# Performance work log

Measured on AMD Instinct MI355X. Metric: run time of the kernel, lower is better.

## Reference

```python
import jax, jax.numpy as jnp
import numpy as np

B, C, H, W = 8, 96, 96, 96
K = 3          # attn_kernels == kernels
HK = 3         # hidden_kernels
NORM_SCALE = 1.0
EPS = 1e-5


def conv2d_same(x, w):
    # x: [B,Cin,H,W], w: [Cout,Cin,k,k], same padding (k odd)
    k = w.shape[-1]
    p = k // 2
    return jax.lax.conv_general_dilated(
        x, w, window_strides=(1, 1), padding=((p, p), (p, p)),
        dimension_numbers=("NCHW", "OIHW", "NCHW"))


def batchnorm_train(x):
    # torch BatchNorm2d (affine=False), training-mode: biased var over (B,H,W)
    mu = jnp.mean(x, axis=(0, 2, 3), keepdims=True)
    var = jnp.var(x, axis=(0, 2, 3), keepdims=True)
    return (x - mu) * jax.lax.rsqrt(var + EPS)


def unfold_nonoverlap(t, k):
    # nn.Unfold(k, stride=k): [B,C,H,W] -> [B, C*k*k, L], L=(H//k)*(W//k)
    b, c, h, w = t.shape
    nh, nw = h // k, w // k
    t = t.reshape(b, c, nh, k, nw, k).transpose(0, 1, 3, 5, 2, 4)  # B,C,kh,kw,nh,nw
    return t.reshape(b, c * k * k, nh * nw)


def unfold_overlap(t, k):
    # nn.Unfold(k, padding=k//2, stride=1): [B,C,H,W] -> [B, C*k*k, H*W]
    b, c, h, w = t.shape
    p = k // 2
    tp = jnp.pad(t, ((0, 0), (0, 0), (p, p), (p, p)))
    views = [tp[:, :, i:i + h, j:j + w] for i in range(k) for j in range(k)]
    return jnp.stack(views, axis=2).reshape(b, c * k * k, h * w)


def attn_conv2d(x, wa1, wa2, wa3, k):
    # x: [B, 2C, H, W]; convs: 2C -> C
    q = conv2d_same(x, wa1)
    kk = conv2d_same(x, wa2)
    v = conv2d_same(x, wa3)
    b, c, h, w = q.shape
    y1 = unfold_nonoverlap(q, k).reshape(b, c, k * k, -1).transpose(0, 2, 1, 3)   # [B,k2,C,L]
    y2 = unfold_nonoverlap(kk, k).reshape(b, c, k * k, -1).transpose(0, 2, 3, 1)  # [B,k2,L,C]
    attn = jnp.matmul(y1, y2)                      # [B,k2,C,C]
    attn = attn.transpose(0, 3, 2, 1)              # [B,C,C,k2]  (torch transpose(1,3))
    attn = attn.reshape(b, c, c * k * k) / np.sqrt(c * k * k)
    attn = jax.nn.softmax(attn, axis=2)            # [B,C,C*k2]
    v_unf = unfold_overlap(v, k)                   # [B,C*k2,H*W]
    out = jnp.matmul(attn, v_unf)                  # [B,C,H*W]
    return out.reshape(b, c, h, w)


def setup_inputs() -> dict:
    key = jax.random.key(0)
    ks = jax.random.split(key, 7)
    s_c = 1.0 / np.sqrt(C * HK * HK)
    s_2c = 1.0 / np.sqrt(2 * C * HK * HK)
    return {
        "x1": jax.random.normal(ks[0], (B, C, H, W), jnp.float32),
        "x2": jax.random.normal(ks[1], (B, C, H, W), jnp.float32),
        "w1": jax.random.normal(ks[2], (C, C, K, K), jnp.float32) * s_c,
        "w2": jax.random.normal(ks[3], (C, C, K, K), jnp.float32) * s_c,
        "wa1": jax.random.normal(ks[4], (C, 2 * C, HK, HK), jnp.float32) * s_2c,
        "wa2": jax.random.normal(ks[5], (C, 2 * C, HK, HK), jnp.float32) * s_2c,
        "wa3": jax.random.normal(ks[6], (C, 2 * C, HK, HK), jnp.float32) * s_2c,
    }


def reference(x1, x2, w1, w2, wa1, wa2, wa3):
    y1 = conv2d_same(x1, w1)
    y2 = conv2d_same(x2, w2)
    x = jnp.concatenate([x1, x2], axis=1)          # [B,2C,H,W]
    y3 = attn_conv2d(x, wa1, wa2, wa3, K)          # [B,C,H,W]
    gated = (NORM_SCALE * batchnorm_train(y1)) * (NORM_SCALE * batchnorm_train(y2))
    y = jnp.concatenate([gated, NORM_SCALE * batchnorm_train(y3)], axis=1)
    return (x + y, x)
```

## Files before the change

kernel.cpp:

```cpp
#include <hip/hip_runtime.h>

#define B_    8
#define C_    96
#define H_    96
#define W_    96
#define HW_   9216
#define CHW_  884736
#define BCHW_ 7077888
#define OUTHALF_ 14155776
#define PAD_  98

typedef __attribute__((ext_vector_type(8))) short short8;
typedef __attribute__((ext_vector_type(4))) float f32x4;

__device__ __forceinline__ unsigned short f2bf(float f) {
    unsigned u = __builtin_bit_cast(unsigned, f);
    u = (u + 0x7FFFu + ((u >> 16) & 1u)) >> 16;
    return (unsigned short)u;
}
__device__ __forceinline__ float bf2f(unsigned short h) {
    return __builtin_bit_cast(float, (unsigned)h << 16);
}

__device__ __forceinline__ void gll16(const void* g, void* l) {
    __builtin_amdgcn_global_load_lds((const __attribute__((address_space(1))) void*)g,
                                     (__attribute__((address_space(3))) void*)l, 16, 0, 0);
}

__global__ __launch_bounds__(256) void pack_x_kernel(
    const float* __restrict__ x1, const float* __restrict__ x2,
    unsigned short* __restrict__ xb, unsigned short* __restrict__ vb)
{
    __shared__ unsigned short lds[192*100];
    const int tid = threadIdx.x;
    const int yp = blockIdx.x;
    const int b  = blockIdx.y;
    if (yp == 98) {
        unsigned short* vbb = vb + (size_t)b*PAD_*PAD_*96;
        for (int i = tid; i < 2*9408; i += 256) {
            int r = (i < 9408) ? 0 : 97;
            int o = (i < 9408) ? i : i - 9408;
            vbb[((size_t)r*PAD_)*96 + o] = 0;
        }
        for (int i = tid; i < 96*192; i += 256) {
            int y = 1 + (i / 192);
            int rem = i % 192;
            int side = rem / 96;
            int c = rem % 96;
            vbb[((size_t)y*PAD_ + side*97)*96 + c] = 0;
        }
        return;
    }
    unsigned short* row = xb + ((size_t)(b*PAD_) + yp)*PAD_*192;
    if (yp == 0 || yp == PAD_-1) {
        for (int i = tid; i < PAD_*192; i += 256) row[i] = 0;
        return;
    }
    const int y = yp - 1;
    for (int i = tid; i < 2*HW_; i += 256) {
        const float* src = (i < HW_) ? x1 : x2;
        int ii = (i < HW_) ? i : i - HW_;
        int ch = ii / 96, x = ii - ch*96;
        int c = (i < HW_) ? ch : ch + 96;
        lds[c*100 + x] = f2bf(src[((size_t)(b*96 + ch))*HW_ + y*96 + x]);
    }
    __syncthreads();
    for (int i = tid; i < PAD_*192; i += 256) {
        int xp = i / 192, c = i - xp*192;
        row[i] = (xp == 0 || xp == PAD_-1) ? (unsigned short)0 : lds[c*100 + (xp-1)];
    }
}

__global__ __launch_bounds__(256) void pack_w_all_kernel(
    const float* __restrict__ w1, const float* __restrict__ w2,
    const float* __restrict__ wa1, const float* __restrict__ wa2,
    const float* __restrict__ wa3,
    unsigned short* __restrict__ wf1, unsigned short* __restrict__ wf2,
    unsigned short* __restrict__ wfa1, unsigned short* __restrict__ wfa2,
    unsigned short* __restrict__ wfa3)
{
    int i = blockIdx.x*256 + threadIdx.x;
    const float* w; unsigned short* wf; int cin, rel;
    if      (i < 82944)  { w = w1;  wf = wf1;  cin = 96;  rel = i; }
    else if (i < 165888) { w = w2;  wf = wf2;  cin = 96;  rel = i - 82944; }
    else if (i < 331776) { w = wa1; wf = wfa1; cin = 192; rel = i - 165888; }
    else if (i < 497664) { w = wa2; wf = wfa2; cin = 192; rel = i - 331776; }
    else                 { w = wa3; wf = wfa3; cin = 192; rel = i - 497664; }
    int j = rel & 7;
    int lane = (rel >> 3) & 63;
    int blk = rel >> 9;
    int mf = blk % 6;
    int step = blk / 6;
    int chunk = step / 9, tap = step - chunk*9;
    int kh = tap / 3, kw = tap - kh*3;
    int m = lane & 15, g = lane >> 4;
    int co = mf*16 + m;
    int ci = chunk*32 + g*8 + j;
    wf[rel] = f2bf(w[(((size_t)co*cin + ci)*3 + kh)*3 + kw]);
}

struct ConvJobs {
    const unsigned short* xin[5];
    const unsigned short* wf[5];
    unsigned short* out[5];
    int chunks[5];
    int ci0[5];
    int mode[5];
    int wstride[5];
    int cistr[5];
};

__global__ __launch_bounds__(256, 2) void conv_mfma_kernel(ConvJobs j)
{
    __shared__ __align__(16) unsigned short xs[2][352*32];
    const int tid  = threadIdx.x;
    const int lane = tid & 63;
    const int wid  = tid >> 6;
    const int wm   = wid & 1;
    const int wp   = wid >> 1;
    const int x0 = blockIdx.x*32, y0 = blockIdx.y*8;
    const int which = blockIdx.z >> 3, b = blockIdx.z & 7;
    const int CHUNKS = j.chunks[which];
    const int CISTR  = j.cistr[which];
    const int ci0_base = j.ci0[which];
    const int NSTEP = CHUNKS*9;
    const unsigned short* xbb = j.xin[which] + (size_t)b*PAD_*PAD_*CISTR;
    const unsigned short* wfb = j.wf[which] + (size_t)b*j.wstride[which];

    auto stage = [&](int chunk, int buf) {
        int ci0 = ci0_base + chunk*32;
        for (int r = wid; r < 22; r += 4) {
            int gi = r*64 + lane;
            int pos = gi >> 2; if (pos > 339) pos = 339;
            int g = gi & 3;
            int gsrc = (g ^ pos) & 3;
            int ty = pos / 34, tx = pos - ty*34;
            gll16(xbb + ((size_t)(y0 + ty)*PAD_ + (x0 + tx))*CISTR + ci0 + gsrc*8,
                  &xs[buf][r*512]);
        }
    };
    auto loadWd = [&](int step, short8* dst) {
        const unsigned short* wstep = wfb + (size_t)step*3072;
        dst[0] = *(const short8*)(wstep + ((wm*3+0)*64 + lane)*8);
        dst[1] = *(const short8*)(wstep + ((wm*3+1)*64 + lane)*8);
        dst[2] = *(const short8*)(wstep + ((wm*3+2)*64 + lane)*8);
    };

    f32x4 acc[3][8];
    f32x4 zero = {0.f, 0.f, 0.f, 0.f};
#pragma unroll
    for (int a = 0; a < 3; ++a)
#pragma unroll
        for (int f = 0; f < 8; ++f) acc[a][f] = zero;

    short8 wq[3][3];
    loadWd(0, wq[0]);
    loadWd(1 < NSTEP ? 1 : 0, wq[1]);
    loadWd(2 < NSTEP ? 2 : 0, wq[2]);
    stage(0, 0);
    __syncthreads();

    for (int chunk = 0; chunk < CHUNKS; ++chunk) {
        const int cur = chunk & 1;
        if (chunk + 1 < CHUNKS) stage(chunk + 1, cur ^ 1);
#pragma unroll
        for (int tap = 0; tap < 9; ++tap) {
            const int step = chunk*9 + tap;
            const int slot = tap % 3;
            short8 wa0 = wq[slot][0], wa1 = wq[slot][1], wa2 = wq[slot][2];
            int pf = step + 3; if (pf >= NSTEP) pf = NSTEP - 1;
            loadWd(pf, wq[slot]);
            const int kh = tap / 3, kw = tap - kh*3;
            const int n = lane & 15, gw = lane >> 4;
#pragma unroll
            for (int r = 0; r < 4; ++r) {
#pragma unroll
                for (int xh = 0; xh < 2; ++xh) {
                    int pos = (wp*4 + r + kh)*34 + (xh*16 + n + kw);
                    int g = (gw ^ pos) & 3;
                    short8 bfrag = *(const short8*)(&xs[cur][pos*32 + g*8]);
                    acc[0][r*2+xh] = __builtin_amdgcn_mfma_f32_16x16x32_bf16(wa0, bfrag, acc[0][r*2+xh], 0, 0, 0);
                    acc[1][r*2+xh] = __builtin_amdgcn_mfma_f32_16x16x32_bf16(wa1, bfrag, acc[1][r*2+xh], 0, 0, 0);
                    acc[2][r*2+xh] = __builtin_amdgcn_mfma_f32_16x16x32_bf16(wa2, bfrag, acc[2][r*2+xh], 0, 0, 0);
                }
            }
        }
        __syncthreads();
    }

    int n = lane & 15, gw = lane >> 4;
    if (j.mode[which] == 1) {
        unsigned short* out = j.out[which];
#pragma unroll
        for (int a = 0; a < 3; ++a)
#pragma unroll
        for (int r = 0; r < 4; ++r)
#pragma unroll
        for (int xh = 0; xh < 2; ++xh) {
            int y = y0 + wp*4 + r, x = x0 + xh*16 + n;
#pragma unroll
            for (int reg = 0; reg < 4; ++reg) {
                int co = wm*48 + a*16 + gw*4 + reg;
                out[((size_t)(b*96 + co))*HW_ + y*96 + x] = f2bf(acc[a][r*2+xh][reg]);
            }
        }
    } else {
        unsigned short* out = j.out[which];
#pragma unroll
        for (int a = 0; a < 3; ++a)
#pragma unroll
        for (int r = 0; r < 4; ++r)
#pragma unroll
        for (int xh = 0; xh < 2; ++xh) {
            int y = y0 + wp*4 + r, x = x0 + xh*16 + n;
            int cb = wm*48 + a*16 + gw*4;
            f32x4 v = acc[a][r*2+xh];
            uint2 pv;
            pv.x = (unsigned)f2bf(v[0]) | ((unsigned)f2bf(v[1]) << 16);
            pv.y = (unsigned)f2bf(v[2]) | ((unsigned)f2bf(v[3]) << 16);
            *(uint2*)(out + ((size_t)(b*PAD_ + y+1)*PAD_ + (x+1))*96 + cb) = pv;
        }
    }
}

__global__ __launch_bounds__(256) void repack_qk_kernel(
    const unsigned short* __restrict__ qb, const unsigned short* __restrict__ kb,
    unsigned short* __restrict__ qt, unsigned short* __restrict__ kt)
{
    __shared__ unsigned short q_lds[HW_], k_lds[HW_];
    const int tid = threadIdx.x;
    const int ch = blockIdx.x, b = blockIdx.y;
    const unsigned short* qsrc = qb + ((size_t)(b*96 + ch))*HW_;
    const unsigned short* ksrc = kb + ((size_t)(b*96 + ch))*HW_;
    for (int i = tid; i < HW_/8; i += 256) {
        *(short8*)(&q_lds[i*8]) = *(const short8*)(qsrc + i*8);
        *(short8*)(&k_lds[i*8]) = *(const short8*)(ksrc + i*8);
    }
    __syncthreads();
    const int l0 = tid*4;
    const int i0 = l0 >> 5, j0 = l0 & 31;
    for (int tap = 0; tap < 9; ++tap) {
        int kh = tap/3, kw = tap - kh*3;
        int base = (3*i0 + kh)*96 + kw;
        ushort4 vq, vk;
        vq.x = q_lds[base + 3*(j0+0)]; vq.y = q_lds[base + 3*(j0+1)];
        vq.z = q_lds[base + 3*(j0+2)]; vq.w = q_lds[base + 3*(j0+3)];
        vk.x = k_lds[base + 3*(j0+0)]; vk.y = k_lds[base + 3*(j0+1)];
        vk.z = k_lds[base + 3*(j0+2)]; vk.w = k_lds[base + 3*(j0+3)];
        size_t dst = (((size_t)(b*9 + tap))*96 + ch)*1024 + l0;
        *(ushort4*)(qt + dst) = vq;
        *(ushort4*)(kt + dst) = vk;
    }
}

__global__ __launch_bounds__(256) void attn_mfma_kernel(
    const unsigned short* __restrict__ qt, const unsigned short* __restrict__ kt,
    float* __restrict__ attnp)
{
    __shared__ __align__(16) unsigned short qs[6144], ks[6144];
    const int tid = threadIdx.x, lane = tid & 63, wid = tid >> 6;
    const int tap = blockIdx.x, b = blockIdx.y, s = blockIdx.z;
    const int wm = wid & 1, wn = wid >> 1;
    const unsigned short* qbase = qt + ((size_t)(b*9 + tap))*96*1024;
    const unsigned short* kbase = kt + ((size_t)(b*9 + tap))*96*1024;

    f32x4 acc[3][3];
    f32x4 zero = {0.f, 0.f, 0.f, 0.f};
#pragma unroll
    for (int i = 0; i < 3; ++i)
#pragma unroll
        for (int j = 0; j < 3; ++j) acc[i][j] = zero;

    const int lrow = lane >> 3, lgr = lane & 7;
    for (int kc = 0; kc < 4; ++kc) {
        int L0 = s*256 + kc*64;
        for (int r = wid; r < 12; r += 4) {
            int row = r*8 + lrow;
            int gsrc = lgr ^ (row & 7);
            gll16(qbase + (size_t)row*1024 + L0 + gsrc*8, &qs[r*512]);
        }
        for (int r = wid; r < 12; r += 4) {
            int row = r*8 + lrow;
            int gsrc = lgr ^ (row & 7);
            gll16(kbase + (size_t)row*1024 + L0 + gsrc*8, &ks[r*512]);
        }
        __syncthreads();
#pragma unroll
        for (int ks_ = 0; ks_ < 2; ++ks_) {
            short8 av[3], bv[3];
#pragma unroll
            for (int am = 0; am < 3; ++am) {
                int row = wm*48 + am*16 + (lane & 15);
                int gp = (ks_*4 + (lane >> 4)) ^ (row & 7);
                av[am] = *(const short8*)(&qs[row*64 + gp*8]);
            }
#pragma unroll
            for (int bn = 0; bn < 3; ++bn) {
                int row = wn*48 + bn*16 + (lane & 15);
                int gp = (ks_*4 + (lane >> 4)) ^ (row & 7);
                bv[bn] = *(const short8*)(&ks[row*64 + gp*8]);
            }
#pragma unroll
            for (int am = 0; am < 3; ++am)
#pragma unroll
                for (int bn = 0; bn < 3; ++bn)
                    acc[am][bn] = __builtin_amdgcn_mfma_f32_16x16x32_bf16(av[am], bv[bn], acc[am][bn], 0, 0, 0);
        }
        __syncthreads();
    }
    float* dst = attnp + ((((size_t)s*8 + b)*9 + tap))*9216;
#pragma unroll
    for (int am = 0; am < 3; ++am)
#pragma unroll
    for (int bn = 0; bn < 3; ++bn)
#pragma unroll
    for (int reg = 0; reg < 4; ++reg) {
        int cq = wm*48 + am*16 + (lane>>4)*4 + reg;
        int ck = wn*48 + bn*16 + (lane&15);
        dst[(size_t)cq*96 + ck] = acc[am][bn][reg];
    }
}

__global__ __launch_bounds__(256) void softmax_kernel(
    const float* __restrict__ attnp, unsigned short* __restrict__ wfab)
{
    __shared__ float red[256];
    const int tid = threadIdx.x;
    const int ck = blockIdx.x % 96, b = blockIdx.x / 96;
    const float scale = 0.03402069087198858f;
    float v[4];
#pragma unroll
    for (int r = 0; r < 4; ++r) {
        int m = r*256 + tid;
        if (m < 864) {
            int cq = m / 9, tap = m - cq*9;
            const float* ap = attnp + ((((size_t)b*9 + tap))*96 + cq)*96 + ck;
            v[r] = (ap[0] + ap[663552] + ap[2*663552] + ap[3*663552]) * scale;
        } else v[r] = -1e30f;
    }
    float mx = fmaxf(fmaxf(v[0], v[1]), fmaxf(v[2], v[3]));
    red[tid] = mx; __syncthreads();
    for (int s = 128; s > 0; s >>= 1) {
        if (tid < s) red[tid] = fmaxf(red[tid], red[tid+s]);
        __syncthreads();
    }
    mx = red[0]; __syncthreads();
    float e[4]; float lsum = 0.f;
#pragma unroll
    for (int r = 0; r < 4; ++r) {
        int m = r*256 + tid;
        if (m < 864) { e[r] = __expf(v[r] - mx); lsum += e[r]; }
        else e[r] = 0.f;
    }
    red[tid] = lsum; __syncthreads();
    for (int s = 128; s > 0; s >>= 1) {
        if (tid < s) red[tid] += red[tid+s];
        __syncthreads();
    }
    float inv = 1.f / red[0];
#pragma unroll
    for (int r = 0; r < 4; ++r) {
        int m = r*256 + tid;
        if (m < 864) {
            int cq = m / 9, tap = m - cq*9;
            int chunk = cq >> 5, cl = cq & 31, g = cl >> 3, j = cl & 7;
            int mf = ck >> 4, mrem = ck & 15;
            int lane2 = mrem + (g << 4);
            size_t oidx = (size_t)b*82944
                + ((((size_t)(chunk*9 + tap)*6 + mf)*64 + lane2)*8 + j);
            wfab[oidx] = f2bf(e[r]*inv);
        }
    }
}

__global__ __launch_bounds__(256) void bn_stats_kernel(
    const unsigned short* __restrict__ y1, const unsigned short* __restrict__ y2,
    const unsigned short* __restrict__ y3, float* __restrict__ stats)
{
    __shared__ float rs[256], rq[256];
    const int tid = threadIdx.x;
    const int t = blockIdx.x / 96, c = blockIdx.x % 96;
    const unsigned short* src = (t == 0) ? y1 : ((t == 1) ? y2 : y3);
    float s = 0.f, q2 = 0.f;
    for (int i = tid; i < 18432; i += 256) {
        int b = i / 2304, qd = i - b*2304;
        ushort4 v4 = *(const ushort4*)(src + ((size_t)(b*96 + c))*HW_ + qd*4);
        float f0 = bf2f(v4.x), f1 = bf2f(v4.y), f2v = bf2f(v4.z), f3 = bf2f(v4.w);
        s += f0+f1+f2v+f3; q2 += f0*f0+f1*f1+f2v*f2v+f3*f3;
    }
    rs[tid] = s; rq[tid] = q2; __syncthreads();
    for (int st = 128; st > 0; st >>= 1) {
        if (tid < st) { rs[tid] += rs[tid+st]; rq[tid] += rq[tid+st]; }
        __syncthreads();
    }
    if (tid == 0) {
        const float nn = 73728.f;
        float mu = rs[0] / nn;
        float var = rq[0] / nn - mu*mu;
        stats[blockIdx.x] = mu;
        stats[288 + blockIdx.x] = rsqrtf(var + 1e-5f);
    }
}

__global__ __launch_bounds__(256) void final_kernel(
    const float* __restrict__ x1, const float* __restrict__ x2,
    const unsigned short* __restrict__ y1, const unsigned short* __restrict__ y2,
    const unsigned short* __restrict__ y3, const float* __restrict__ stats,
    float* __restrict__ out)
{
    size_t q4 = (size_t)blockIdx.x*256 + threadIdx.x;
    size_t base = q4*4;
    int b  = (int)(base / CHW_);
    int c  = (int)((base / HW_) % 96);
    int hw = (int)(base % HW_);
    float mu1 = stats[c],       r1 = stats[288 + c];
    float mu2 = stats[96 + c],  r2 = stats[384 + c];
    float mu3 = stats[192 + c], r3 = stats[480 + c];
    float4 x1v = *(const float4*)(x1 + base);
    float4 x2v = *(const float4*)(x2 + base);
    ushort4 a1 = *(const ushort4*)(y1 + base);
    ushort4 a2 = *(const ushort4*)(y2 + base);
    ushort4 a3 = *(const ushort4*)(y3 + base);
    size_t lo = ((size_t)(b*192 + c))*HW_ + hw;
    size_t hi = lo + (size_t)96*HW_;
    float4 o0, o1;
    o0.x = x1v.x + ((bf2f(a1.x)-mu1)*r1) * ((bf2f(a2.x)-mu2)*r2);
    o0.y = x1v.y + ((bf2f(a1.y)-mu1)*r1) * ((bf2f(a2.y)-mu2)*r2);
    o0.z = x1v.z + ((bf2f(a1.z)-mu1)*r1) * ((bf2f(a2.z)-mu2)*r2);
    o0.w = x1v.w + ((bf2f(a1.w)-mu1)*r1) * ((bf2f(a2.w)-mu2)*r2);
    o1.x = x2v.x + (bf2f(a3.x)-mu3)*r3;
    o1.y = x2v.y + (bf2f(a3.y)-mu3)*r3;
    o1.z = x2v.z + (bf2f(a3.z)-mu3)*r3;
    o1.w = x2v.w + (bf2f(a3.w)-mu3)*r3;
    *(float4*)(out + lo) = o0;
    *(float4*)(out + hi) = o1;
    *(float4*)(out + OUTHALF_ + lo) = x1v;
    *(float4*)(out + OUTHALF_ + hi) = x2v;
}

extern "C" void kernel_launch(void* const* d_in, const int* in_sizes, int n_in,
                              void* d_out, int out_size, void* d_ws, size_t ws_size,
                              hipStream_t stream)
{
    const float* x1  = (const float*)d_in[0];
    const float* x2  = (const float*)d_in[1];
    const float* w1  = (const float*)d_in[2];
    const float* w2  = (const float*)d_in[3];
    const float* wa1 = (const float*)d_in[4];
    const float* wa2 = (const float*)d_in[5];
    const float* wa3 = (const float*)d_in[6];
    float* out = (float*)d_out;
    char* ws = (char*)d_ws;

    unsigned short* xb   = (unsigned short*)(ws);
    unsigned short* y1b  = (unsigned short*)(ws + 29503488);
    unsigned short* y2b  = (unsigned short*)(ws + 43659264);
    unsigned short* y3b  = (unsigned short*)(ws + 57815040);
    unsigned short* wf1  = (unsigned short*)(ws + 71970816);
    unsigned short* wf2  = (unsigned short*)(ws + 72136704);
    unsigned short* wfa1 = (unsigned short*)(ws + 72302592);
    unsigned short* wfa2 = (unsigned short*)(ws + 72634368);
    unsigned short* wfa3 = (unsigned short*)(ws + 72966144);
    unsigned short* wfab = (unsigned short*)(ws + 73297920);
    float* stats = (float*)(ws + 74625024);

    unsigned short* qb    = (unsigned short*)out;
    unsigned short* kkb   = (unsigned short*)((char*)out + 14155776);
    unsigned short* vb    = (unsigned short*)((char*)out + 28311552);
    unsigned short* qt    = (unsigned short*)((char*)out + 43063296);
    unsigned short* kt    = (unsigned short*)((char*)out + 57219072);
    float*          attnp = (float*)((char*)out + 71374848);

    pack_w_all_kernel<<<2592, 256, 0, stream>>>(w1, w2, wa1, wa2, wa3,
                                                wf1, wf2, wfa1, wfa2, wfa3);
    pack_x_kernel<<<dim3(99, 8), 256, 0, stream>>>(x1, x2, xb, vb);

    ConvJobs jA;
    jA.xin[0]=xb;  jA.wf[0]=wfa1; jA.out[0]=qb;  jA.chunks[0]=6; jA.ci0[0]=0;  jA.mode[0]=1; jA.wstride[0]=0; jA.cistr[0]=192;
    jA.xin[1]=xb;  jA.wf[1]=wfa2; jA.out[1]=kkb; jA.chunks[1]=6; jA.ci0[1]=0;  jA.mode[1]=1; jA.wstride[1]=0; jA.cistr[1]=192;
    jA.xin[2]=xb;  jA.wf[2]=wfa3; jA.out[2]=vb;  jA.chunks[2]=6; jA.ci0[2]=0;  jA.mode[2]=2; jA.wstride[2]=0; jA.cistr[2]=192;
    jA.xin[3]=xb;  jA.wf[3]=wf1;  jA.out[3]=y1b; jA.chunks[3]=3; jA.ci0[3]=0;  jA.mode[3]=1; jA.wstride[3]=0; jA.cistr[3]=192;
    jA.xin[4]=xb;  jA.wf[4]=wf2;  jA.out[4]=y2b; jA.chunks[4]=3; jA.ci0[4]=96; jA.mode[4]=1; jA.wstride[4]=0; jA.cistr[4]=192;
    conv_mfma_kernel<<<dim3(3, 12, 40), 256, 0, stream>>>(jA);

    repack_qk_kernel<<<dim3(96, 8), 256, 0, stream>>>(qb, kkb, qt, kt);
    attn_mfma_kernel<<<dim3(9, 8, 4), 256, 0, stream>>>(qt, kt, attnp);
    softmax_kernel<<<768, 256, 0, stream>>>(attnp, wfab);

    ConvJobs jB;
    for (int s = 0; s < 5; ++s) {
        jB.xin[s]=vb; jB.wf[s]=wfab; jB.out[s]=y3b; jB.chunks[s]=3; jB.ci0[s]=0;
        jB.mode[s]=1; jB.wstride[s]=82944; jB.cistr[s]=96;
    }
    conv_mfma_kernel<<<dim3(3, 12, 8), 256, 0, stream>>>(jB);

    bn_stats_kernel<<<288, 256, 0, stream>>>(y1b, y2b, y3b, stats);
    final_kernel<<<6912, 256, 0, stream>>>(x1, x2, y1b, y2b, y3b, stats, out);
}
```

Baseline: 237.4 us.

## Fuse BatchNorm statistics into conv epilogue and halve conv row tile

BatchNorm sum and sum-of-squares are now accumulated in the conv kernel's epilogue with wavefront shuffles, LDS atomics and global atomics, which removes the separate bn_stats pass that re-read y1/y2/y3. The final kernel computes mean and rsqrt from the raw sums, and pack_w zeroes the accumulators. The conv tile also shrinks from 8 to 4 rows, with a smaller LDS buffer and launch bounds raised to 4 blocks per SM, giving twice as many blocks and higher occupancy. The cost is more halo reloads per output and the float atomic adds, whose order varies, so the statistics can differ slightly from run to run.

New measurement: 280.1 us. +18.0%, slower.

```diff
diff --git a/kernel.cpp b/kernel.cpp
--- a/kernel.cpp
+++ b/kernel.cpp
@@ -77,9 +77,10 @@
     const float* __restrict__ wa3,
     unsigned short* __restrict__ wf1, unsigned short* __restrict__ wf2,
     unsigned short* __restrict__ wfa1, unsigned short* __restrict__ wfa2,
-    unsigned short* __restrict__ wfa3)
+    unsigned short* __restrict__ wfa3, float* __restrict__ stats_raw)
 {
     int i = blockIdx.x*256 + threadIdx.x;
+    if (i < 576) stats_raw[i] = 0.f;
     const float* w; unsigned short* wf; int cin, rel;
     if      (i < 82944)  { w = w1;  wf = wf1;  cin = 96;  rel = i; }
     else if (i < 165888) { w = w2;  wf = wf2;  cin = 96;  rel = i - 82944; }
@@ -108,17 +109,19 @@
     int mode[5];
     int wstride[5];
     int cistr[5];
+    int dobn[5];
+    int bnslot[5];
 };
 
-__global__ __launch_bounds__(256, 2) void conv_mfma_kernel(ConvJobs j)
-{
-    __shared__ __align__(16) unsigned short xs[2][352*32];
+__global__ __launch_bounds__(256, 4) void conv_mfma_kernel(ConvJobs j, float* __restrict__ stats_raw)
+{
+    __shared__ __align__(16) unsigned short xs[2][6656];
     const int tid  = threadIdx.x;
     const int lane = tid & 63;
     const int wid  = tid >> 6;
     const int wm   = wid & 1;
     const int wp   = wid >> 1;
-    const int x0 = blockIdx.x*32, y0 = blockIdx.y*8;
+    const int x0 = blockIdx.x*32, y0 = blockIdx.y*4;
     const int which = blockIdx.z >> 3, b = blockIdx.z & 7;
     const int CHUNKS = j.chunks[which];
     const int CISTR  = j.cistr[which];
@@ -129,9 +132,9 @@
 
     auto stage = [&](int chunk, int buf) {
         int ci0 = ci0_base + chunk*32;
-        for (int r = wid; r < 22; r += 4) {
+        for (int r = wid; r < 13; r += 4) {
             int gi = r*64 + lane;
-            int pos = gi >> 2; if (pos > 339) pos = 339;
+            int pos = gi >> 2; if (pos > 203) pos = 203;
             int g = gi & 3;
             int gsrc = (g ^ pos) & 3;
             int ty = pos / 34, tx = pos - ty*34;
@@ -146,12 +149,12 @@
         dst[2] = *(const short8*)(wstep + ((wm*3+2)*64 + lane)*8);
     };
 
-    f32x4 acc[3][8];
+    f32x4 acc[3][4];
     f32x4 zero = {0.f, 0.f, 0.f, 0.f};
 #pragma unroll
     for (int a = 0; a < 3; ++a)
 #pragma unroll
-        for (int f = 0; f < 8; ++f) acc[a][f] = zero;
+        for (int f = 0; f < 4; ++f) acc[a][f] = zero;
 
     short8 wq[3][3];
     loadWd(0, wq[0]);
@@ -173,10 +176,10 @@
             const int kh = tap / 3, kw = tap - kh*3;
             const int n = lane & 15, gw = lane >> 4;
 #pragma unroll
-            for (int r = 0; r < 4; ++r) {
+            for (int r = 0; r < 2; ++r) {
 #pragma unroll
                 for (int xh = 0; xh < 2; ++xh) {
-                    int pos = (wp*4 + r + kh)*34 + (xh*16 + n + kw);
+                    int pos = (wp*2 + r + kh)*34 + (xh*16 + n + kw);
                     int g = (gw ^ pos) & 3;
                     short8 bfrag = *(const short8*)(&xs[cur][pos*32 + g*8]);
                     acc[0][r*2+xh] = __builtin_amdgcn_mfma_f32_16x16x32_bf16(wa0, bfrag, acc[0][r*2+xh], 0, 0, 0);
@@ -188,16 +191,16 @@
         __syncthreads();
     }
 
-    int n = lane & 15, gw = lane >> 4;
+    const int n = lane & 15, gw = lane >> 4;
     if (j.mode[which] == 1) {
         unsigned short* out = j.out[which];
 #pragma unroll
         for (int a = 0; a < 3; ++a)
 #pragma unroll
-        for (int r = 0; r < 4; ++r)
+        for (int r = 0; r < 2; ++r)
 #pragma unroll
         for (int xh = 0; xh < 2; ++xh) {
-            int y = y0 + wp*4 + r, x = x0 + xh*16 + n;
+            int y = y0 + wp*2 + r, x = x0 + xh*16 + n;
 #pragma unroll
             for (int reg = 0; reg < 4; ++reg) {
                 int co = wm*48 + a*16 + gw*4 + reg;
@@ -209,16 +212,47 @@
 #pragma unroll
         for (int a = 0; a < 3; ++a)
 #pragma unroll
-        for (int r = 0; r < 4; ++r)
+        for (int r = 0; r < 2; ++r)
 #pragma unroll
         for (int xh = 0; xh < 2; ++xh) {
-            int y = y0 + wp*4 + r, x = x0 + xh*16 + n;
+            int y = y0 + wp*2 + r, x = x0 + xh*16 + n;
             int cb = wm*48 + a*16 + gw*4;
             f32x4 v = acc[a][r*2+xh];
             uint2 pv;
             pv.x = (unsigned)f2bf(v[0]) | ((unsigned)f2bf(v[1]) << 16);
             pv.y = (unsigned)f2bf(v[2]) | ((unsigned)f2bf(v[3]) << 16);
             *(uint2*)(out + ((size_t)(b*PAD_ + y+1)*PAD_ + (x+1))*96 + cb) = pv;
+        }
+    }
+
+    if (j.dobn[which]) {
+        float* lds_s = (float*)&xs[0][0];
+        float* lds_q = lds_s + 96;
+        if (tid < 192) lds_s[tid] = 0.f;
+        __syncthreads();
+#pragma unroll
+        for (int a = 0; a < 3; ++a)
+#pragma unroll
+        for (int reg = 0; reg < 4; ++reg) {
+            float s = 0.f, q2 = 0.f;
+#pragma unroll
+            for (int f = 0; f < 4; ++f) { float v = acc[a][f][reg]; s += v; q2 += v*v; }
+#pragma unroll
+            for (int m = 1; m < 16; m <<= 1) {
+                s  += __shfl_xor(s, m);
+                q2 += __shfl_xor(q2, m);
+            }
+            if (n == 0) {
+                int co = wm*48 + a*16 + gw*4 + reg;
+                atomicAdd(&lds_s[co], s);
+                atomicAdd(&lds_q[co], q2);
+            }
+        }
+        __syncthreads();
+        if (tid < 96) {
+            int t = j.bnslot[which];
+            atomicAdd(stats_raw + t*96 + tid, lds_s[tid]);
+            atomicAdd(stats_raw + 288 + t*96 + tid, lds_q[tid]);
         }
     }
 }
@@ -373,39 +407,10 @@
     }
 }
 
-__global__ __launch_bounds__(256) void bn_stats_kernel(
-    const unsigned short* __restrict__ y1, const unsigned short* __restrict__ y2,
-    const unsigned short* __restrict__ y3, float* __restrict__ stats)
-{
-    __shared__ float rs[256], rq[256];
-    const int tid = threadIdx.x;
-    const int t = blockIdx.x / 96, c = blockIdx.x % 96;
-    const unsigned short* src = (t == 0) ? y1 : ((t == 1) ? y2 : y3);
-    float s = 0.f, q2 = 0.f;
-    for (int i = tid; i < 18432; i += 256) {
-        int b = i / 2304, qd = i - b*2304;
-        ushort4 v4 = *(const ushort4*)(src + ((size_t)(b*96 + c))*HW_ + qd*4);
-        float f0 = bf2f(v4.x), f1 = bf2f(v4.y), f2v = bf2f(v4.z), f3 = bf2f(v4.w);
-        s += f0+f1+f2v+f3; q2 += f0*f0+f1*f1+f2v*f2v+f3*f3;
-    }
-    rs[tid] = s; rq[tid] = q2; __syncthreads();
-    for (int st = 128; st > 0; st >>= 1) {
-        if (tid < st) { rs[tid] += rs[tid+st]; rq[tid] += rq[tid+st]; }
-        __syncthreads();
-    }
-    if (tid == 0) {
-        const float nn = 73728.f;
-        float mu = rs[0] / nn;
-        float var = rq[0] / nn - mu*mu;
-        stats[blockIdx.x] = mu;
-        stats[288 + blockIdx.x] = rsqrtf(var + 1e-5f);
-    }
-}
-
 __global__ __launch_bounds__(256) void final_kernel(
     const float* __restrict__ x1, const float* __restrict__ x2,
     const unsigned short* __restrict__ y1, const unsigned short* __restrict__ y2,
-    const unsigned short* __restrict__ y3, const float* __restrict__ stats,
+    const unsigned short* __restrict__ y3, const float* __restrict__ stats_raw,
     float* __restrict__ out)
 {
     size_t q4 = (size_t)blockIdx.x*256 + threadIdx.x;
@@ -413,9 +418,14 @@
     int b  = (int)(base / CHW_);
     int c  = (int)((base / HW_) % 96);
     int hw = (int)(base % HW_);
-    float mu1 = stats[c],       r1 = stats[288 + c];
-    float mu2 = stats[96 + c],  r2 = stats[384 + c];
-    float mu3 = stats[192 + c], r3 = stats[480 + c];
+    const float NN = 73728.f;
+    float s1 = stats_raw[c],        qq1 = stats_raw[288 + c];
+    float s2 = stats_raw[96 + c],   qq2 = stats_raw[384 + c];
+    float s3 = stats_raw[192 + c],  qq3 = stats_raw[480 + c];
+    float mu1 = s1/NN, mu2 = s2/NN, mu3 = s3/NN;
+    float r1 = rsqrtf(qq1/NN - mu1*mu1 + 1e-5f);
+    float r2 = rsqrtf(qq2/NN - mu2*mu2 + 1e-5f);
+    float r3 = rsqrtf(qq3/NN - mu3*mu3 + 1e-5f);
     float4 x1v = *(const float4*)(x1 + base);
     float4 x2v = *(const float4*)(x2 + base);
     ushort4 a1 = *(const ushort4*)(y1 + base);
@@ -462,7 +472,7 @@
     unsigned short* wfa2 = (unsigned short*)(ws + 72634368);
     unsigned short* wfa3 = (unsigned short*)(ws + 72966144);
     unsigned short* wfab = (unsigned short*)(ws + 73297920);
-    float* stats = (float*)(ws + 74625024);
+    float* stats_raw = (float*)(ws + 74625024);
 
     unsigned short* qb    = (unsigned short*)out;
     unsigned short* kkb   = (unsigned short*)((char*)out + 14155776);
@@ -472,16 +482,17 @@
     float*          attnp = (float*)((char*)out + 71374848);
 
     pack_w_all_kernel<<<2592, 256, 0, stream>>>(w1, w2, wa1, wa2, wa3,
-                                                wf1, wf2, wfa1, wfa2, wfa3);
+                                                wf1, wf2, wfa1, wfa2, wfa3,
+                                                stats_raw);
     pack_x_kernel<<<dim3(99, 8), 256, 0, stream>>>(x1, x2, xb, vb);
 
     ConvJobs jA;
-    jA.xin[0]=xb;  jA.wf[0]=wfa1; jA.out[0]=qb;  jA.chunks[0]=6; jA.ci0[0]=0;  jA.mode[0]=1; jA.wstride[0]=0; jA.cistr[0]=192;
-    jA.xin[1]=xb;  jA.wf[1]=wfa2; jA.out[1]=kkb; jA.chunks[1]=6; jA.ci0[1]=0;  jA.mode[1]=1; jA.wstride[1]=0; jA.cistr[1]=192;
-    jA.xin[2]=xb;  jA.wf[2]=wfa3; jA.out[2]=vb;  jA.chunks[2]=6; jA.ci0[2]=0;  jA.mode[2]=2; jA.wstride[2]=0; jA.cistr[2]=192;
-    jA.xin[3]=xb;  jA.wf[3]=wf1;  jA.out[3]=y1b; jA.chunks[3]=3; jA.ci0[3]=0;  jA.mode[3]=1; jA.wstride[3]=0; jA.cistr[3]=192;
-    jA.xin[4]=xb;  jA.wf[4]=wf2;  jA.out[4]=y2b; jA.chunks[4]=3; jA.ci0[4]=96; jA.mode[4]=1; jA.wstride[4]=0; jA.cistr[4]=192;
-    conv_mfma_kernel<<<dim3(3, 12, 40), 256, 0, stream>>>(jA);
+    jA.xin[0]=xb;  jA.wf[0]=wfa1; jA.out[0]=qb;  jA.chunks[0]=6; jA.ci0[0]=0;  jA.mode[0]=1; jA.wstride[0]=0; jA.cistr[0]=192; jA.dobn[0]=0; jA.bnslot[0]=0;
+    jA.xin[1]=xb;  jA.wf[1]=wfa2; jA.out[1]=kkb; jA.chunks[1]=6; jA.ci0[1]=0;  jA.mode[1]=1; jA.wstride[1]=0; jA.cistr[1]=192; jA.dobn[1]=0; jA.bnslot[1]=0;
+    jA.xin[2]=xb;  jA.wf[2]=wfa3; jA.out[2]=vb;  jA.chunks[2]=6; jA.ci0[2]=0;  jA.mode[2]=2; jA.wstride[2]=0; jA.cistr[2]=192; jA.dobn[2]=0; jA.bnslot[2]=0;
+    jA.xin[3]=xb;  jA.wf[3]=wf1;  jA.out[3]=y1b; jA.chunks[3]=3; jA.ci0[3]=0;  jA.mode[3]=1; jA.wstride[3]=0; jA.cistr[3]=192; jA.dobn[3]=1; jA.bnslot[3]=0;
+    jA.xin[4]=xb;  jA.wf[4]=wf2;  jA.out[4]=y2b; jA.chunks[4]=3; jA.ci0[4]=96; jA.mode[4]=1; jA.wstride[4]=0; jA.cistr[4]=192; jA.dobn[4]=1; jA.bnslot[4]=1;
+    conv_mfma_kernel<<<dim3(3, 24, 40), 256, 0, stream>>>(jA, stats_raw);
 
     repack_qk_kernel<<<dim3(96, 8), 256, 0, stream>>>(qb, kkb, qt, kt);
     attn_mfma_kernel<<<dim3(9, 8, 4), 256, 0, stream>>>(qt, kt, attnp);
@@ -490,10 +501,9 @@
     ConvJobs jB;
     for (int s = 0; s < 5; ++s) {
         jB.xin[s]=vb; jB.wf[s]=wfab; jB.out[s]=y3b; jB.chunks[s]=3; jB.ci0[s]=0;
-        jB.mode[s]=1; jB.wstride[s]=82944; jB.cistr[s]=96;
-    }
-    conv_mfma_kernel<<<dim3(3, 12, 8), 256, 0, stream>>>(jB);
-
-    bn_stats_kernel<<<288, 256, 0, stream>>>(y1b, y2b, y3b, stats);
-    final_kernel<<<6912, 256, 0, stream>>>(x1, x2, y1b, y2b, y3b, stats, out);
-}
+        jB.mode[s]=1; jB.wstride[s]=82944; jB.cistr[s]=96; jB.dobn[s]=1; jB.bnslot[s]=2;
+    }
+    conv_mfma_kernel<<<dim3(3, 24, 8), 256, 0, stream>>>(jB, stats_raw);
+
+    final_kernel<<<6912, 256, 0, stream>>>(x1, x2, y1b, y2b, y3b, stats_raw, out);
+}
```
